# Kernel tuning notes

Measured on AMD Instinct MI355X. Metric: run time of the kernel, lower is better.

Reference implementation:

```python
import jax, jax.numpy as jnp
import numpy as np

STRIDES = (8, 16, 32)
FEAT_SIZES = ((160, 160), (80, 80), (40, 40))
NUM_CLASSES = 1
NUM_KPTS = 17
PRE_TOP_K = 1000


def _priors_and_strides():
    """MlvlPointGenerator.grid_priors with offset=0 (YOLOX convention)."""
    priors, strides = [], []
    for (h, w), s in zip(FEAT_SIZES, STRIDES):
        yy, xx = jnp.meshgrid(jnp.arange(h, dtype=jnp.float32),
                              jnp.arange(w, dtype=jnp.float32), indexing='ij')
        priors.append(jnp.stack([xx.reshape(-1) * s, yy.reshape(-1) * s], axis=-1))
        strides.append(jnp.full((h * w,), float(s), dtype=jnp.float32))
    return jnp.concatenate(priors, 0), jnp.concatenate(strides, 0)  # (N,2), (N,)


def _flat(x, c):
    # (B,C,H,W) -> (B,H*W,c)
    b = x.shape[0]
    return jnp.transpose(x, (0, 2, 3, 1)).reshape(b, -1, c)


def setup_inputs() -> dict:
    key = jax.random.key(0)
    ks = jax.random.split(key, 15)
    names_chans = [('cls', NUM_CLASSES), ('bbox', 4), ('obj', 1),
                   ('kpt', 2 * NUM_KPTS), ('vis', NUM_KPTS)]
    inp = {}
    i = 0
    for name, c in names_chans:
        for lvl, (h, w) in enumerate(FEAT_SIZES):
            inp[f'{name}{lvl}'] = jax.random.normal(ks[i], (32, c, h, w), dtype=jnp.float32)
            i += 1
    return inp


def reference(cls0, cls1, cls2, bbox0, bbox1, bbox2, obj0, obj1, obj2,
              kpt0, kpt1, kpt2, vis0, vis1, vis2):
    priors, stride = _priors_and_strides()  # (N,2), (N,)
    B = cls0.shape[0]

    cls_s = jnp.concatenate([_flat(x, NUM_CLASSES) for x in (cls0, cls1, cls2)], 1)
    bbox_p = jnp.concatenate([_flat(x, 4) for x in (bbox0, bbox1, bbox2)], 1)
    obj_s = jnp.concatenate([_flat(x, 1).squeeze(-1) for x in (obj0, obj1, obj2)], 1)
    kpt_p = jnp.concatenate([_flat(x, 2 * NUM_KPTS) for x in (kpt0, kpt1, kpt2)], 1)
    vis_p = jnp.concatenate([_flat(x, NUM_KPTS) for x in (vis0, vis1, vis2)], 1)

    scores = jax.nn.sigmoid(cls_s) * jax.nn.sigmoid(obj_s)[..., None]  # (B,N,C)
    vis = jax.nn.sigmoid(vis_p)                                        # (B,N,K)

    # YOLOXBBoxCoder.decode
    s = stride[None, :, None]
    xys = bbox_p[..., :2] * s + priors[None]
    whs = jnp.exp(bbox_p[..., 2:]) * s
    half = whs * 0.5
    bboxes = jnp.concatenate([xys - half, xys + half], axis=-1)  # (B,N,4)

    # decode_pose: offsets (B,N,K,2) * stride + grid
    kpts = kpt_p.reshape(B, -1, NUM_KPTS, 2) * stride[None, :, None, None] \
        + priors[:, None, :][None]                                # (B,N,K,2)
    pred_kpts = jnp.concatenate([kpts, vis[..., None]], axis=3)   # (B,N,K,3)

    max_scores = jnp.max(scores, axis=-1)                         # (B,N)
    _, keep = jax.lax.top_k(max_scores, PRE_TOP_K)                # (B,pre_top_k)

    dets = jnp.concatenate([bboxes, scores], axis=2)              # (B,N,4+C)
    dets = jnp.take_along_axis(dets, keep[:, :, None], axis=1)
    pred_kpts = jnp.take_along_axis(pred_kpts, keep[:, :, None, None], axis=1)
    return dets, pred_kpts
```

## Files before the change

### kernel.cpp

```cpp
#include <hip/hip_runtime.h>
#include <stdint.h>
#include <math.h>

#define BATCH 32
#define NANCH 33600
#define N0 25600
#define N1 6400
#define N2 1600
#define TOPK 1000
#define NBIN 4096
#define CCAP 2816

__device__ __forceinline__ float sigmoid_np(float x) {
    float e = (float)::exp(-(double)x);
    return 1.0f / (1.0f + e);
}

__global__ void score_kernel(const float* __restrict__ cls0, const float* __restrict__ cls1,
                             const float* __restrict__ cls2,
                             const float* __restrict__ obj0, const float* __restrict__ obj1,
                             const float* __restrict__ obj2,
                             float* __restrict__ S) {
    int n = blockIdx.x * blockDim.x + threadIdx.x;
    int b = blockIdx.y;
    if (n >= NANCH) return;
    const float* cp; const float* op; int nl;
    if (n < N0)            { cp = cls0 + (size_t)b * N0; op = obj0 + (size_t)b * N0; nl = n; }
    else if (n < N0 + N1)  { cp = cls1 + (size_t)b * N1; op = obj1 + (size_t)b * N1; nl = n - N0; }
    else                   { cp = cls2 + (size_t)b * N2; op = obj2 + (size_t)b * N2; nl = n - N0 - N1; }
    S[(size_t)b * NANCH + n] = sigmoid_np(cp[nl]) * sigmoid_np(op[nl]);
}

__global__ __launch_bounds__(1024) void select_kernel(const float* __restrict__ S_g,
                                                      int* __restrict__ keep) {
    const int b = blockIdx.x;
    const float* S = S_g + (size_t)b * NANCH;
    __shared__ unsigned hist[NBIN];
    __shared__ unsigned scan[1024];
    __shared__ unsigned long long wbuf[TOPK];
    __shared__ unsigned long long cbuf[CCAP];
    __shared__ unsigned sh_T, sh_above, sh_d, sh_k2, wcnt, ccnt;
    const int tid = threadIdx.x;

    if (tid == 0) { wcnt = 0u; ccnt = 0u; }
    for (int i = tid; i < NBIN; i += 1024) hist[i] = 0u;
    __syncthreads();

    const float4* S4 = (const float4*)S;
    const int M4 = NANCH / 4;
    for (int i = tid; i < M4; i += 1024) {
        float4 v = S4[i];
        atomicAdd(&hist[__float_as_uint(v.x) >> 19], 1u);
        atomicAdd(&hist[__float_as_uint(v.y) >> 19], 1u);
        atomicAdd(&hist[__float_as_uint(v.z) >> 19], 1u);
        atomicAdd(&hist[__float_as_uint(v.w) >> 19], 1u);
    }
    __syncthreads();

    unsigned s0 = hist[4 * tid + 0], s1 = hist[4 * tid + 1];
    unsigned s2 = hist[4 * tid + 2], s3 = hist[4 * tid + 3];
    unsigned tot = s0 + s1 + s2 + s3;
    scan[tid] = tot;
    __syncthreads();
    for (int off = 1; off < 1024; off <<= 1) {
        unsigned v = scan[tid] + ((tid + off < 1024) ? scan[tid + off] : 0u);
        __syncthreads();
        scan[tid] = v;
        __syncthreads();
    }
    unsigned excl = scan[tid] - tot;
    {
        unsigned a3 = excl,        f3 = excl + s3;
        unsigned a2 = f3,          f2 = f3 + s2;
        unsigned a1 = f2,          f1 = f2 + s1;
        unsigned a0 = f1,          f0 = f1 + s0;
        if (a3 < TOPK && f3 >= TOPK) { sh_T = 4u * tid + 3u; sh_above = a3; }
        if (a2 < TOPK && f2 >= TOPK) { sh_T = 4u * tid + 2u; sh_above = a2; }
        if (a1 < TOPK && f1 >= TOPK) { sh_T = 4u * tid + 1u; sh_above = a1; }
        if (a0 < TOPK && f0 >= TOPK) { sh_T = 4u * tid + 0u; sh_above = a0; }
    }
    __syncthreads();
    const unsigned T = sh_T;
    const unsigned above = sh_above;
    const unsigned need = TOPK - above;

    for (int i = tid; i < M4; i += 1024) {
        float4 v = S4[i];
        float c[4] = {v.x, v.y, v.z, v.w};
        #pragma unroll
        for (int q = 0; q < 4; ++q) {
            unsigned u = __float_as_uint(c[q]);
            unsigned bin = u >> 19;
            if (bin >= T) {
                unsigned n = (unsigned)(4 * i + q);
                unsigned long long key = ((unsigned long long)u << 32)
                                       | (unsigned long long)(0xFFFFFFFFu - n);
                if (bin > T) {
                    unsigned p = atomicAdd(&wcnt, 1u);
                    wbuf[p] = key;
                } else {
                    unsigned p = atomicAdd(&ccnt, 1u);
                    if (p < CCAP) cbuf[p] = key;
                }
            }
        }
    }
    __syncthreads();

    if (ccnt <= CCAP) {
        const int W = (int)wcnt;
        if (tid < W) {
            unsigned long long my = wbuf[tid];
            int r = 0;
            for (int j = 0; j < W; ++j) r += (wbuf[j] > my) ? 1 : 0;
            keep[b * TOPK + r] = (int)(0xFFFFFFFFu - (unsigned)(my & 0xFFFFFFFFULL));
        }
        const int C = (int)ccnt;
        if (tid < C) {
            unsigned long long my = cbuf[tid];
            int r = 0;
            for (int j = 0; j < C; ++j) r += (cbuf[j] > my) ? 1 : 0;
            if (r < (int)need)
                keep[b * TOPK + W + r] = (int)(0xFFFFFFFFu - (unsigned)(my & 0xFFFFFFFFULL));
        }
    } else {
        unsigned long long prefix = 0ULL;
        unsigned k = TOPK;
        for (int pass = 7; pass >= 0; --pass) {
            if (tid < 256) hist[tid] = 0u;
            __syncthreads();
            const int shift = pass * 8;
            const unsigned long long prefmask =
                (pass == 7) ? 0ULL : (0xFFFFFFFFFFFFFFFFULL << (shift + 8));
            for (int i = tid; i < NANCH; i += 1024) {
                unsigned u = __float_as_uint(S[i]);
                unsigned long long key = ((unsigned long long)u << 32)
                                       | (unsigned long long)(0xFFFFFFFFu - (unsigned)i);
                if ((key & prefmask) == prefix)
                    atomicAdd(&hist[(unsigned)((key >> shift) & 0xFFULL)], 1u);
            }
            __syncthreads();
            if (tid == 0) {
                unsigned cum = 0; int d = 0;
                for (int v = 255; v >= 0; --v) {
                    unsigned c = hist[v];
                    if (cum + c >= k) { d = v; break; }
                    cum += c;
                }
                sh_d = (unsigned)d;
                sh_k2 = k - cum;
            }
            __syncthreads();
            prefix |= ((unsigned long long)sh_d) << shift;
            k = sh_k2;
            __syncthreads();
        }
        if (tid == 0) wcnt = 0u;
        __syncthreads();
        for (int i = tid; i < NANCH; i += 1024) {
            unsigned u = __float_as_uint(S[i]);
            unsigned long long key = ((unsigned long long)u << 32)
                                   | (unsigned long long)(0xFFFFFFFFu - (unsigned)i);
            if (key >= prefix) {
                unsigned pos = atomicAdd(&wcnt, 1u);
                wbuf[pos] = key;
            }
        }
        __syncthreads();
        const int m = (int)wcnt;
        if (tid < m) {
            unsigned long long my = wbuf[tid];
            int r = 0;
            for (int j = 0; j < m; ++j) r += (wbuf[j] > my) ? 1 : 0;
            keep[b * TOPK + r] = (int)(0xFFFFFFFFu - (unsigned)(my & 0xFFFFFFFFULL));
        }
    }
}

__global__ void emit_kernel(const int* __restrict__ keep,
                            const float* __restrict__ S,
                            const float* __restrict__ bbox0, const float* __restrict__ bbox1,
                            const float* __restrict__ bbox2,
                            const float* __restrict__ kpt0, const float* __restrict__ kpt1,
                            const float* __restrict__ kpt2,
                            const float* __restrict__ vis0, const float* __restrict__ vis1,
                            const float* __restrict__ vis2,
                            float* __restrict__ out) {
    int gid = blockIdx.x * blockDim.x + threadIdx.x;
    const int total = BATCH * TOPK * 18;
    if (gid >= total) return;
    int slot = gid % 18;
    int br   = gid / 18;
    int r = br % TOPK;
    int b = br / TOPK;
    int n = keep[b * TOPK + r];

    int nl, W, HW; float s;
    const float *bb, *kp, *vp;
    if (n < N0) {
        nl = n;            W = 160; HW = N0; s = 8.f;
        bb = bbox0; kp = kpt0; vp = vis0;
    } else if (n < N0 + N1) {
        nl = n - N0;       W = 80;  HW = N1; s = 16.f;
        bb = bbox1; kp = kpt1; vp = vis1;
    } else {
        nl = n - N0 - N1;  W = 40;  HW = N2; s = 32.f;
        bb = bbox2; kp = kpt2; vp = vis2;
    }
    float px = (float)(nl % W) * s;
    float py = (float)(nl / W) * s;

    if (slot == 17) {
        float bx = bb[((size_t)b * 4 + 0) * HW + nl];
        float by = bb[((size_t)b * 4 + 1) * HW + nl];
        float bw = bb[((size_t)b * 4 + 2) * HW + nl];
        float bh = bb[((size_t)b * 4 + 3) * HW + nl];
        float score = S[(size_t)b * NANCH + n];
        float cx = bx * s + px;
        float cy = by * s + py;
        float hw_ = expf(bw) * s * 0.5f;
        float hh  = expf(bh) * s * 0.5f;
        float* o = out + ((size_t)b * TOPK + r) * 5;
        o[0] = cx - hw_;
        o[1] = cy - hh;
        o[2] = cx + hw_;
        o[3] = cy + hh;
        o[4] = score;
    } else {
        int kk = slot;
        float xk = kp[((size_t)b * 34 + 2 * kk    ) * HW + nl];
        float yk = kp[((size_t)b * 34 + 2 * kk + 1) * HW + nl];
        float vv = vp[((size_t)b * 17 + kk        ) * HW + nl];
        float* o = out + (size_t)(BATCH * TOPK * 5) + (((size_t)b * TOPK + r) * 17 + kk) * 3;
        o[0] = xk * s + px;
        o[1] = yk * s + py;
        o[2] = sigmoid_np(vv);
    }
}

extern "C" void kernel_launch(void* const* d_in, const int* in_sizes, int n_in,
                              void* d_out, int out_size, void* d_ws, size_t ws_size,
                              hipStream_t stream) {
    const float* cls0  = (const float*)d_in[0];
    const float* cls1  = (const float*)d_in[1];
    const float* cls2  = (const float*)d_in[2];
    const float* bbox0 = (const float*)d_in[3];
    const float* bbox1 = (const float*)d_in[4];
    const float* bbox2 = (const float*)d_in[5];
    const float* obj0  = (const float*)d_in[6];
    const float* obj1  = (const float*)d_in[7];
    const float* obj2  = (const float*)d_in[8];
    const float* kpt0  = (const float*)d_in[9];
    const float* kpt1  = (const float*)d_in[10];
    const float* kpt2  = (const float*)d_in[11];
    const float* vis0  = (const float*)d_in[12];
    const float* vis1  = (const float*)d_in[13];
    const float* vis2  = (const float*)d_in[14];
    float* out = (float*)d_out;

    float* S  = (float*)d_ws;
    int* keep = (int*)((char*)d_ws + (size_t)BATCH * NANCH * sizeof(float));

    dim3 g1((NANCH + 255) / 256, BATCH);
    score_kernel<<<g1, 256, 0, stream>>>(cls0, cls1, cls2, obj0, obj1, obj2, S);

    select_kernel<<<BATCH, 1024, 0, stream>>>(S, keep);

    const int total = BATCH * TOPK * 18;
    emit_kernel<<<(total + 255) / 256, 256, 0, stream>>>(keep, S,
        bbox0, bbox1, bbox2, kpt0, kpt1, kpt2, vis0, vis1, vis2, out);
}
```

Before: 299.6 us.

## Move histogram into score kernel and emit via anchor-order sweep with rank map

The score kernel now builds the per-batch 4096-bin histogram with global atomics, so the select kernel only reads it instead of rescanning scores. Selection writes a per-anchor rank map instead of a keep list. A new sweep kernel walks anchors in order, skips wavefronts with no selected anchors, and gathers bbox/keypoint channels with coalesced-ish reads in place of random gathers. The cost is an extra init kernel clearing a 4 MB rank array, global atomic contention on the histogram, and a scattered 51-float write per kept anchor.

Result: slower. 418.3 us (+39.6%).

```diff
diff --git a/kernel.cpp b/kernel.cpp
--- a/kernel.cpp
+++ b/kernel.cpp
@@ -10,17 +10,24 @@
 #define TOPK 1000
 #define NBIN 4096
 #define CCAP 2816
+#define DETS_SIZE (BATCH * TOPK * 5)
 
 __device__ __forceinline__ float sigmoid_np(float x) {
     float e = (float)::exp(-(double)x);
     return 1.0f / (1.0f + e);
+}
+
+__global__ void init_kernel(int* __restrict__ rank, unsigned* __restrict__ ghist) {
+    int i = blockIdx.x * blockDim.x + threadIdx.x;
+    if (i < BATCH * NANCH) rank[i] = -1;
+    if (i < BATCH * NBIN) ghist[i] = 0u;
 }
 
 __global__ void score_kernel(const float* __restrict__ cls0, const float* __restrict__ cls1,
                              const float* __restrict__ cls2,
                              const float* __restrict__ obj0, const float* __restrict__ obj1,
                              const float* __restrict__ obj2,
-                             float* __restrict__ S) {
+                             float* __restrict__ S, unsigned* __restrict__ ghist) {
     int n = blockIdx.x * blockDim.x + threadIdx.x;
     int b = blockIdx.y;
     if (n >= NANCH) return;
@@ -28,14 +35,16 @@
     if (n < N0)            { cp = cls0 + (size_t)b * N0; op = obj0 + (size_t)b * N0; nl = n; }
     else if (n < N0 + N1)  { cp = cls1 + (size_t)b * N1; op = obj1 + (size_t)b * N1; nl = n - N0; }
     else                   { cp = cls2 + (size_t)b * N2; op = obj2 + (size_t)b * N2; nl = n - N0 - N1; }
-    S[(size_t)b * NANCH + n] = sigmoid_np(cp[nl]) * sigmoid_np(op[nl]);
+    float sc = sigmoid_np(cp[nl]) * sigmoid_np(op[nl]);
+    S[(size_t)b * NANCH + n] = sc;
+    atomicAdd(&ghist[(size_t)b * NBIN + (__float_as_uint(sc) >> 19)], 1u);
 }
 
 __global__ __launch_bounds__(1024) void select_kernel(const float* __restrict__ S_g,
-                                                      int* __restrict__ keep) {
+                                                      const unsigned* __restrict__ ghist,
+                                                      int* __restrict__ rank) {
     const int b = blockIdx.x;
     const float* S = S_g + (size_t)b * NANCH;
-    __shared__ unsigned hist[NBIN];
     __shared__ unsigned scan[1024];
     __shared__ unsigned long long wbuf[TOPK];
     __shared__ unsigned long long cbuf[CCAP];
@@ -43,22 +52,10 @@
     const int tid = threadIdx.x;
 
     if (tid == 0) { wcnt = 0u; ccnt = 0u; }
-    for (int i = tid; i < NBIN; i += 1024) hist[i] = 0u;
-    __syncthreads();
-
-    const float4* S4 = (const float4*)S;
-    const int M4 = NANCH / 4;
-    for (int i = tid; i < M4; i += 1024) {
-        float4 v = S4[i];
-        atomicAdd(&hist[__float_as_uint(v.x) >> 19], 1u);
-        atomicAdd(&hist[__float_as_uint(v.y) >> 19], 1u);
-        atomicAdd(&hist[__float_as_uint(v.z) >> 19], 1u);
-        atomicAdd(&hist[__float_as_uint(v.w) >> 19], 1u);
-    }
-    __syncthreads();
-
-    unsigned s0 = hist[4 * tid + 0], s1 = hist[4 * tid + 1];
-    unsigned s2 = hist[4 * tid + 2], s3 = hist[4 * tid + 3];
+    unsigned s0 = ghist[(size_t)b * NBIN + 4 * tid + 0];
+    unsigned s1 = ghist[(size_t)b * NBIN + 4 * tid + 1];
+    unsigned s2 = ghist[(size_t)b * NBIN + 4 * tid + 2];
+    unsigned s3 = ghist[(size_t)b * NBIN + 4 * tid + 3];
     unsigned tot = s0 + s1 + s2 + s3;
     scan[tid] = tot;
     __syncthreads();
@@ -70,10 +67,10 @@
     }
     unsigned excl = scan[tid] - tot;
     {
-        unsigned a3 = excl,        f3 = excl + s3;
-        unsigned a2 = f3,          f2 = f3 + s2;
-        unsigned a1 = f2,          f1 = f2 + s1;
-        unsigned a0 = f1,          f0 = f1 + s0;
+        unsigned a3 = excl,      f3 = excl + s3;
+        unsigned a2 = f3,        f2 = f3 + s2;
+        unsigned a1 = f2,        f1 = f2 + s1;
+        unsigned a0 = f1,        f0 = f1 + s0;
         if (a3 < TOPK && f3 >= TOPK) { sh_T = 4u * tid + 3u; sh_above = a3; }
         if (a2 < TOPK && f2 >= TOPK) { sh_T = 4u * tid + 2u; sh_above = a2; }
         if (a1 < TOPK && f1 >= TOPK) { sh_T = 4u * tid + 1u; sh_above = a1; }
@@ -84,6 +81,8 @@
     const unsigned above = sh_above;
     const unsigned need = TOPK - above;
 
+    const float4* S4 = (const float4*)S;
+    const int M4 = NANCH / 4;
     for (int i = tid; i < M4; i += 1024) {
         float4 v = S4[i];
         float c[4] = {v.x, v.y, v.z, v.w};
@@ -113,21 +112,24 @@
             unsigned long long my = wbuf[tid];
             int r = 0;
             for (int j = 0; j < W; ++j) r += (wbuf[j] > my) ? 1 : 0;
-            keep[b * TOPK + r] = (int)(0xFFFFFFFFu - (unsigned)(my & 0xFFFFFFFFULL));
+            unsigned n = 0xFFFFFFFFu - (unsigned)(my & 0xFFFFFFFFULL);
+            rank[(size_t)b * NANCH + n] = r;
         }
         const int C = (int)ccnt;
         if (tid < C) {
             unsigned long long my = cbuf[tid];
             int r = 0;
             for (int j = 0; j < C; ++j) r += (cbuf[j] > my) ? 1 : 0;
-            if (r < (int)need)
-                keep[b * TOPK + W + r] = (int)(0xFFFFFFFFu - (unsigned)(my & 0xFFFFFFFFULL));
+            if (r < (int)need) {
+                unsigned n = 0xFFFFFFFFu - (unsigned)(my & 0xFFFFFFFFULL);
+                rank[(size_t)b * NANCH + n] = (int)above + r;
+            }
         }
     } else {
         unsigned long long prefix = 0ULL;
         unsigned k = TOPK;
         for (int pass = 7; pass >= 0; --pass) {
-            if (tid < 256) hist[tid] = 0u;
+            if (tid < 256) scan[tid] = 0u;
             __syncthreads();
             const int shift = pass * 8;
             const unsigned long long prefmask =
@@ -137,13 +139,13 @@
                 unsigned long long key = ((unsigned long long)u << 32)
                                        | (unsigned long long)(0xFFFFFFFFu - (unsigned)i);
                 if ((key & prefmask) == prefix)
-                    atomicAdd(&hist[(unsigned)((key >> shift) & 0xFFULL)], 1u);
+                    atomicAdd(&scan[(unsigned)((key >> shift) & 0xFFULL)], 1u);
             }
             __syncthreads();
             if (tid == 0) {
                 unsigned cum = 0; int d = 0;
                 for (int v = 255; v >= 0; --v) {
-                    unsigned c = hist[v];
+                    unsigned c = scan[v];
                     if (cum + c >= k) { d = v; break; }
                     cum += c;
                 }
@@ -172,50 +174,49 @@
             unsigned long long my = wbuf[tid];
             int r = 0;
             for (int j = 0; j < m; ++j) r += (wbuf[j] > my) ? 1 : 0;
-            keep[b * TOPK + r] = (int)(0xFFFFFFFFu - (unsigned)(my & 0xFFFFFFFFULL));
-        }
-    }
-}
-
-__global__ void emit_kernel(const int* __restrict__ keep,
-                            const float* __restrict__ S,
-                            const float* __restrict__ bbox0, const float* __restrict__ bbox1,
-                            const float* __restrict__ bbox2,
-                            const float* __restrict__ kpt0, const float* __restrict__ kpt1,
-                            const float* __restrict__ kpt2,
-                            const float* __restrict__ vis0, const float* __restrict__ vis1,
-                            const float* __restrict__ vis2,
-                            float* __restrict__ out) {
-    int gid = blockIdx.x * blockDim.x + threadIdx.x;
-    const int total = BATCH * TOPK * 18;
-    if (gid >= total) return;
-    int slot = gid % 18;
-    int br   = gid / 18;
-    int r = br % TOPK;
-    int b = br / TOPK;
-    int n = keep[b * TOPK + r];
-
+            unsigned n = 0xFFFFFFFFu - (unsigned)(my & 0xFFFFFFFFULL);
+            rank[(size_t)b * NANCH + n] = r;
+        }
+    }
+}
+
+__global__ __launch_bounds__(256) void sweep_emit(
+        const int* __restrict__ rank_g, const float* __restrict__ S,
+        const float* __restrict__ bbox0, const float* __restrict__ bbox1,
+        const float* __restrict__ bbox2,
+        const float* __restrict__ kpt0, const float* __restrict__ kpt1,
+        const float* __restrict__ kpt2,
+        const float* __restrict__ vis0, const float* __restrict__ vis1,
+        const float* __restrict__ vis2,
+        float* __restrict__ out) {
+    int n = blockIdx.x * 256 + threadIdx.x;
+    int b = blockIdx.y;
+    bool valid = (n < NANCH);
+    int r = valid ? rank_g[(size_t)b * NANCH + n] : -1;
+    if (__ballot(r >= 0) == 0ULL) return;
+
+    int nc = valid ? n : 0;
     int nl, W, HW; float s;
     const float *bb, *kp, *vp;
-    if (n < N0) {
-        nl = n;            W = 160; HW = N0; s = 8.f;
+    if (nc < N0) {
+        nl = nc;            W = 160; HW = N0; s = 8.f;
         bb = bbox0; kp = kpt0; vp = vis0;
-    } else if (n < N0 + N1) {
-        nl = n - N0;       W = 80;  HW = N1; s = 16.f;
+    } else if (nc < N0 + N1) {
+        nl = nc - N0;       W = 80;  HW = N1; s = 16.f;
         bb = bbox1; kp = kpt1; vp = vis1;
     } else {
-        nl = n - N0 - N1;  W = 40;  HW = N2; s = 32.f;
+        nl = nc - N0 - N1;  W = 40;  HW = N2; s = 32.f;
         bb = bbox2; kp = kpt2; vp = vis2;
     }
     float px = (float)(nl % W) * s;
     float py = (float)(nl / W) * s;
 
-    if (slot == 17) {
-        float bx = bb[((size_t)b * 4 + 0) * HW + nl];
-        float by = bb[((size_t)b * 4 + 1) * HW + nl];
-        float bw = bb[((size_t)b * 4 + 2) * HW + nl];
-        float bh = bb[((size_t)b * 4 + 3) * HW + nl];
-        float score = S[(size_t)b * NANCH + n];
+    float score = S[(size_t)b * NANCH + nc];
+    float bx = bb[((size_t)b * 4 + 0) * HW + nl];
+    float by = bb[((size_t)b * 4 + 1) * HW + nl];
+    float bw = bb[((size_t)b * 4 + 2) * HW + nl];
+    float bh = bb[((size_t)b * 4 + 3) * HW + nl];
+    if (r >= 0) {
         float cx = bx * s + px;
         float cy = by * s + py;
         float hw_ = expf(bw) * s * 0.5f;
@@ -226,15 +227,17 @@
         o[2] = cx + hw_;
         o[3] = cy + hh;
         o[4] = score;
-    } else {
-        int kk = slot;
-        float xk = kp[((size_t)b * 34 + 2 * kk    ) * HW + nl];
-        float yk = kp[((size_t)b * 34 + 2 * kk + 1) * HW + nl];
-        float vv = vp[((size_t)b * 17 + kk        ) * HW + nl];
-        float* o = out + (size_t)(BATCH * TOPK * 5) + (((size_t)b * TOPK + r) * 17 + kk) * 3;
-        o[0] = xk * s + px;
-        o[1] = yk * s + py;
-        o[2] = sigmoid_np(vv);
+    }
+    float* ok = out + DETS_SIZE + ((size_t)b * TOPK + (size_t)(r < 0 ? 0 : r)) * 51;
+    for (int k = 0; k < 17; ++k) {
+        float xk = kp[((size_t)b * 34 + 2 * k    ) * HW + nl];
+        float yk = kp[((size_t)b * 34 + 2 * k + 1) * HW + nl];
+        float vv = vp[((size_t)b * 17 + k        ) * HW + nl];
+        if (r >= 0) {
+            ok[3 * k + 0] = xk * s + px;
+            ok[3 * k + 1] = yk * s + py;
+            ok[3 * k + 2] = 1.0f / (1.0f + expf(-vv));
+        }
     }
 }
 
@@ -258,15 +261,19 @@
     const float* vis2  = (const float*)d_in[14];
     float* out = (float*)d_out;
 
-    float* S  = (float*)d_ws;
-    int* keep = (int*)((char*)d_ws + (size_t)BATCH * NANCH * sizeof(float));
+    char* ws = (char*)d_ws;
+    float*    S     = (float*)ws;                                   ws += (size_t)BATCH * NANCH * sizeof(float);
+    int*      rank  = (int*)ws;                                     ws += (size_t)BATCH * NANCH * sizeof(int);
+    unsigned* ghist = (unsigned*)ws;
+
+    const int initN = BATCH * NANCH;
+    init_kernel<<<(initN + 255) / 256, 256, 0, stream>>>(rank, ghist);
 
     dim3 g1((NANCH + 255) / 256, BATCH);
-    score_kernel<<<g1, 256, 0, stream>>>(cls0, cls1, cls2, obj0, obj1, obj2, S);
-
-    select_kernel<<<BATCH, 1024, 0, stream>>>(S, keep);
-
-    const int total = BATCH * TOPK * 18;
-    emit_kernel<<<(total + 255) / 256, 256, 0, stream>>>(keep, S,
+    score_kernel<<<g1, 256, 0, stream>>>(cls0, cls1, cls2, obj0, obj1, obj2, S, ghist);
+
+    select_kernel<<<BATCH, 1024, 0, stream>>>(S, ghist, rank);
+
+    sweep_emit<<<g1, 256, 0, stream>>>(rank, S,
         bbox0, bbox1, bbox2, kpt0, kpt1, kpt2, vis0, vis1, vis2, out);
 }
```
